# Kernel optimization log

Measured on AMD Instinct MI355X. Metric: run time of the kernel, lower is better.

Reference implementation:

```python
import jax, jax.numpy as jnp
import numpy as np

N_NODES = 100000
N_EDGES = 800000
IN_DIM = 128
HIDDEN_DIM = 256
OUT_DIM = 40


def setup_inputs() -> dict:
    key = jax.random.key(0)
    k_x, k_e, k_w1, k_w2 = jax.random.split(key, 4)
    x = jax.random.normal(k_x, (N_NODES, IN_DIM), dtype=jnp.float32)
    edge_index = jax.random.randint(k_e, (2, N_EDGES), 0, N_NODES, dtype=jnp.int32)
    # Glorot-style init like PyG GCNConv
    s1 = 1.0 / np.sqrt(IN_DIM)
    s2 = 1.0 / np.sqrt(HIDDEN_DIM)
    W1 = jax.random.uniform(k_w1, (IN_DIM, HIDDEN_DIM), dtype=jnp.float32, minval=-s1, maxval=s1)
    b1 = jnp.zeros((HIDDEN_DIM,), dtype=jnp.float32)
    W2 = jax.random.uniform(k_w2, (HIDDEN_DIM, OUT_DIM), dtype=jnp.float32, minval=-s2, maxval=s2)
    b2 = jnp.zeros((OUT_DIM,), dtype=jnp.float32)
    return {"x": x, "edge_index": edge_index, "W1": W1, "b1": b1, "W2": W2, "b2": b2}


def _gcn_conv(x, W, b, src, dst, n_nodes):
    # PyG GCNConv: linear transform, add self-loops, symmetric normalization,
    # scatter-add aggregation, then bias.
    h = x @ W  # [N, F_out]
    loops = jnp.arange(n_nodes, dtype=src.dtype)
    s = jnp.concatenate([src, loops])  # [E+N]
    d = jnp.concatenate([dst, loops])
    deg = jax.ops.segment_sum(jnp.ones_like(d, dtype=h.dtype), d, num_segments=n_nodes)
    dinv = jax.lax.rsqrt(jnp.maximum(deg, 1.0))  # deg >= 1 with self-loops
    norm = dinv[s] * dinv[d]  # [E+N]
    msgs = h[s] * norm[:, None]  # [E+N, F_out] -- dominant memory traffic
    out = jax.ops.segment_sum(msgs, d, num_segments=n_nodes)
    return out + b


def reference(x, edge_index, W1, b1, W2, b2):
    src, dst = edge_index[0], edge_index[1]
    n = x.shape[0]
    h = _gcn_conv(x, W1, b1, src, dst, n)
    h = jax.nn.relu(h)
    # dropout is identity in eval mode
    h = _gcn_conv(h, W2, b2, src, dst, n)
    return jax.nn.log_softmax(h, axis=1)
```

## Files before the change

### kernel.cpp

```cpp
#include <hip/hip_runtime.h>
#include <math.h>

#define N_NODES 100000
#define N_EDGES 800000
#define IN_DIM 128
#define HIDDEN_DIM 256
#define OUT_DIM 40
#define CAP 32
#define SHARD_DIV 12500
#define NPAIRS (N_NODES * 64)
#define T1 (HIDDEN_DIM * IN_DIM)
#define T2 (64 * HIDDEN_DIM)
#define CHUNKS 782
#define GROUP 40
#define NBLOCKS (CHUNKS * GROUP)

typedef __attribute__((ext_vector_type(8))) __bf16 bf16x8;
typedef __attribute__((ext_vector_type(4))) float f32x4;

#define FIXSC 131072.0f
#define FIXSC_INV 7.62939453125e-6f

__device__ __forceinline__ unsigned short f2bf(float f) {
    unsigned u = __float_as_uint(f);
    unsigned r = (u + 0x7FFFu + ((u >> 16) & 1u)) >> 16;
    return (unsigned short)r;
}
__device__ __forceinline__ float bflo(unsigned v) { return __uint_as_float(v << 16); }
__device__ __forceinline__ float bfhi(unsigned v) { return __uint_as_float(v & 0xFFFF0000u); }

__device__ __forceinline__ bf16x8 ld_frag16(const unsigned short* p) {
    union { uint4 u; bf16x8 b; } t;
    t.u = *(const uint4*)p;
    return t.b;
}

__global__ __launch_bounds__(256) void fillcast_kernel(const int* __restrict__ src,
                                                       const int* __restrict__ dst,
                                                       int* __restrict__ cnt,
                                                       int* __restrict__ esrc,
                                                       const float* __restrict__ x,
                                                       unsigned* __restrict__ xs,
                                                       const float* __restrict__ W1,
                                                       unsigned short* __restrict__ W1t,
                                                       const float* __restrict__ W2,
                                                       unsigned short* __restrict__ W2f) {
    int bid = blockIdx.x;
    int g = bid / GROUP, r = bid % GROUP;
    if (r < 8) {
        int lo = r * SHARD_DIV;
        int i0 = g * 1024 + threadIdx.x * 4;
        if (i0 + 3 < N_EDGES) {
            int4 d4 = *(const int4*)&dst[i0];
            if ((unsigned)(d4.x - lo) < (unsigned)SHARD_DIV) {
                int p = atomicAdd(&cnt[d4.x], 1);
                if (p < CAP) esrc[d4.x * CAP + p] = src[i0];
            }
            if ((unsigned)(d4.y - lo) < (unsigned)SHARD_DIV) {
                int p = atomicAdd(&cnt[d4.y], 1);
                if (p < CAP) esrc[d4.y * CAP + p] = src[i0 + 1];
            }
            if ((unsigned)(d4.z - lo) < (unsigned)SHARD_DIV) {
                int p = atomicAdd(&cnt[d4.z], 1);
                if (p < CAP) esrc[d4.z * CAP + p] = src[i0 + 2];
            }
            if ((unsigned)(d4.w - lo) < (unsigned)SHARD_DIV) {
                int p = atomicAdd(&cnt[d4.w], 1);
                if (p < CAP) esrc[d4.w * CAP + p] = src[i0 + 3];
            }
        } else {
            for (int j = 0; j < 4; j++) {
                int i = i0 + j;
                if (i < N_EDGES) {
                    int d = dst[i];
                    if ((unsigned)(d - lo) < (unsigned)SHARD_DIV) {
                        int p = atomicAdd(&cnt[d], 1);
                        if (p < CAP) esrc[d * CAP + p] = src[i];
                    }
                }
            }
        }
    } else {
        int ci = g * 32 + (r - 8);
        int i = ci * 256 + threadIdx.x;
        if (i < NPAIRS) {
            float2 v = ((const float2*)x)[i];
            xs[i] = (unsigned)f2bf(v.x * FIXSC) | ((unsigned)f2bf(v.y * FIXSC) << 16);
        }
        if (i < T1) {
            int n = i >> 7, k = i & 127;
            W1t[i] = f2bf(W1[(size_t)k * HIDDEN_DIM + n]);
        } else if (i < T1 + T2) {
            int j = i - T1;
            int e = j & 7, lane = (j >> 3) & 63, frag = j >> 9;
            int l16 = lane & 15, quad = lane >> 4;
            int c2 = frag >> 3, chunk = (frag >> 1) & 3, kk = frag & 1;
            int n = c2 * 16 + l16;
            int k = chunk * 64 + kk * 32 + quad * 8 + e;
            float v = (n < OUT_DIM) ? W2[(size_t)k * OUT_DIM + n] : 0.0f;
            W2f[j] = f2bf(v);
        }
    }
}

__global__ __launch_bounds__(256) void aggx_kernel(const unsigned* __restrict__ xs,
                                                   const int* __restrict__ cnt,
                                                   const int* __restrict__ esrc,
                                                   unsigned* __restrict__ aggxb, int n) {
    int wave = (blockIdx.x * 256 + threadIdx.x) >> 6;
    int lane = threadIdx.x & 63;
    int half = lane >> 5, l32 = lane & 31;
    int node = wave * 2 + half;
    if (node >= n) return;
    int c = cnt[node];
    int m = c < CAP ? c : CAP;
    const uint2* xs2 = (const uint2*)xs;
    float dn = rsqrtf((float)c + 1.0f);
    uint2 v = xs2[(size_t)node * 32 + l32];
    int ia0 = (int)(bflo(v.x) * dn), ib0 = (int)(bfhi(v.x) * dn);
    int ia1 = (int)(bflo(v.y) * dn), ib1 = (int)(bfhi(v.y) * dn);
    int base = node * CAP;
    int j = 0;
    for (; j + 7 < m; j += 8) {
        int4 sa = *(const int4*)&esrc[base + j];
        int4 sb = *(const int4*)&esrc[base + j + 4];
        float d0 = rsqrtf((float)cnt[sa.x] + 1.0f);
        float d1 = rsqrtf((float)cnt[sa.y] + 1.0f);
        float d2 = rsqrtf((float)cnt[sa.z] + 1.0f);
        float d3 = rsqrtf((float)cnt[sa.w] + 1.0f);
        float d4 = rsqrtf((float)cnt[sb.x] + 1.0f);
        float d5 = rsqrtf((float)cnt[sb.y] + 1.0f);
        float d6 = rsqrtf((float)cnt[sb.z] + 1.0f);
        float d7 = rsqrtf((float)cnt[sb.w] + 1.0f);
        uint2 u0 = xs2[(size_t)sa.x * 32 + l32];
        uint2 u1 = xs2[(size_t)sa.y * 32 + l32];
        uint2 u2 = xs2[(size_t)sa.z * 32 + l32];
        uint2 u3 = xs2[(size_t)sa.w * 32 + l32];
        uint2 u4 = xs2[(size_t)sb.x * 32 + l32];
        uint2 u5 = xs2[(size_t)sb.y * 32 + l32];
        uint2 u6 = xs2[(size_t)sb.z * 32 + l32];
        uint2 u7 = xs2[(size_t)sb.w * 32 + l32];
        ia0 += ((int)(bflo(u0.x) * d0) + (int)(bflo(u1.x) * d1)) + ((int)(bflo(u2.x) * d2) + (int)(bflo(u3.x) * d3))
             + ((int)(bflo(u4.x) * d4) + (int)(bflo(u5.x) * d5)) + ((int)(bflo(u6.x) * d6) + (int)(bflo(u7.x) * d7));
        ib0 += ((int)(bfhi(u0.x) * d0) + (int)(bfhi(u1.x) * d1)) + ((int)(bfhi(u2.x) * d2) + (int)(bfhi(u3.x) * d3))
             + ((int)(bfhi(u4.x) * d4) + (int)(bfhi(u5.x) * d5)) + ((int)(bfhi(u6.x) * d6) + (int)(bfhi(u7.x) * d7));
        ia1 += ((int)(bflo(u0.y) * d0) + (int)(bflo(u1.y) * d1)) + ((int)(bflo(u2.y) * d2) + (int)(bflo(u3.y) * d3))
             + ((int)(bflo(u4.y) * d4) + (int)(bflo(u5.y) * d5)) + ((int)(bflo(u6.y) * d6) + (int)(bflo(u7.y) * d7));
        ib1 += ((int)(bfhi(u0.y) * d0) + (int)(bfhi(u1.y) * d1)) + ((int)(bfhi(u2.y) * d2) + (int)(bfhi(u3.y) * d3))
             + ((int)(bfhi(u4.y) * d4) + (int)(bfhi(u5.y) * d5)) + ((int)(bfhi(u6.y) * d6) + (int)(bfhi(u7.y) * d7));
    }
    for (; j + 3 < m; j += 4) {
        int4 s = *(const int4*)&esrc[base + j];
        float d0 = rsqrtf((float)cnt[s.x] + 1.0f);
        float d1 = rsqrtf((float)cnt[s.y] + 1.0f);
        float d2 = rsqrtf((float)cnt[s.z] + 1.0f);
        float d3 = rsqrtf((float)cnt[s.w] + 1.0f);
        uint2 u0 = xs2[(size_t)s.x * 32 + l32];
        uint2 u1 = xs2[(size_t)s.y * 32 + l32];
        uint2 u2 = xs2[(size_t)s.z * 32 + l32];
        uint2 u3 = xs2[(size_t)s.w * 32 + l32];
        ia0 += ((int)(bflo(u0.x) * d0) + (int)(bflo(u1.x) * d1)) + ((int)(bflo(u2.x) * d2) + (int)(bflo(u3.x) * d3));
        ib0 += ((int)(bfhi(u0.x) * d0) + (int)(bfhi(u1.x) * d1)) + ((int)(bfhi(u2.x) * d2) + (int)(bfhi(u3.x) * d3));
        ia1 += ((int)(bflo(u0.y) * d0) + (int)(bflo(u1.y) * d1)) + ((int)(bflo(u2.y) * d2) + (int)(bflo(u3.y) * d3));
        ib1 += ((int)(bfhi(u0.y) * d0) + (int)(bfhi(u1.y) * d1)) + ((int)(bfhi(u2.y) * d2) + (int)(bfhi(u3.y) * d3));
    }
    for (; j < m; j++) {
        int s = esrc[base + j];
        float d = rsqrtf((float)cnt[s] + 1.0f);
        uint2 u = xs2[(size_t)s * 32 + l32];
        ia0 += (int)(bflo(u.x) * d); ib0 += (int)(bfhi(u.x) * d);
        ia1 += (int)(bflo(u.y) * d); ib1 += (int)(bfhi(u.y) * d);
    }
    float k = dn * FIXSC_INV;
    uint2 o;
    o.x = (unsigned)f2bf((float)ia0 * k) | ((unsigned)f2bf((float)ib0 * k) << 16);
    o.y = (unsigned)f2bf((float)ia1 * k) | ((unsigned)f2bf((float)ib1 * k) << 16);
    ((uint2*)aggxb)[(size_t)node * 32 + l32] = o;
}

#define BSTR 136
#define HSTR 72
__device__ __forceinline__ void phase2_epi(f32x4 (&acc)[16], int rowg,
                                           unsigned short* hw,
                                           const unsigned short* __restrict__ W2f,
                                           const float* __restrict__ b1,
                                           const int* __restrict__ cnt,
                                           unsigned short* __restrict__ h2s,
                                           int lane, int quad, int l16, int M) {
    f32x4 acc2[3];
#pragma unroll
    for (int c2 = 0; c2 < 3; c2++) acc2[c2] = (f32x4){0.f, 0.f, 0.f, 0.f};
#pragma unroll
    for (int chunk = 0; chunk < 4; chunk++) {
#pragma unroll
        for (int cc = 0; cc < 4; cc++) {
            int ct = chunk * 4 + cc;
            float bb = b1[ct * 16 + l16];
#pragma unroll
            for (int r = 0; r < 4; r++) {
                int row = quad * 4 + r;
                float v = fmaxf(acc[ct][r] + bb, 0.0f);
                hw[row * HSTR + cc * 16 + l16] = f2bf(v);
            }
        }
#pragma unroll
        for (int kk = 0; kk < 2; kk++) {
            bf16x8 af2 = ld_frag16(&hw[l16 * HSTR + kk * 32 + quad * 8]);
#pragma unroll
            for (int c2 = 0; c2 < 3; c2++) {
                bf16x8 bfr = ld_frag16(&W2f[(size_t)((c2 * 8 + chunk * 2 + kk) * 64 + lane) * 8]);
                acc2[c2] = __builtin_amdgcn_mfma_f32_16x16x32_bf16(af2, bfr, acc2[c2], 0, 0, 0);
            }
        }
    }
#pragma unroll
    for (int c2 = 0; c2 < 3; c2++) {
        int col = c2 * 16 + l16;
#pragma unroll
        for (int r = 0; r < 4; r++) {
            int gm = rowg + quad * 4 + r;
            if (gm < M) {
                float v = acc2[c2][r] * (rsqrtf((float)cnt[gm] + 1.0f) * FIXSC);
                h2s[(size_t)gm * 64 + col] = f2bf(v);
            }
        }
    }
}

__global__ __launch_bounds__(256, 2) void gemm12_kernel(const unsigned short* __restrict__ A,
                                                        const unsigned short* __restrict__ W1t,
                                                        const unsigned short* __restrict__ W2f,
                                                        const float* __restrict__ b1,
                                                        const int* __restrict__ cnt,
                                                        unsigned short* __restrict__ h2s,
                                                        int M) {
    __shared__ __align__(16) unsigned short Bs[256 * BSTR];
    __shared__ __align__(16) unsigned short Hs[4 * 16 * HSTR];
    int tid = threadIdx.x;
    int wv = tid >> 6, lane = tid & 63;
    int quad = lane >> 4, l16 = lane & 15;
    int row0 = blockIdx.x * 128 + wv * 32;

#pragma unroll
    for (int rep = 0; rep < 16; rep++) {
        int lin = rep * 256 + tid;
        int row = lin >> 4, ch = lin & 15;
        *(uint4*)&Bs[row * BSTR + ch * 8] = *(const uint4*)&W1t[(size_t)row * 128 + ch * 8];
    }

    f32x4 zero4 = {0.f, 0.f, 0.f, 0.f};
    f32x4 accA[16], accB[16];
#pragma unroll
    for (int ct = 0; ct < 16; ct++) { accA[ct] = zero4; accB[ct] = zero4; }

    __syncthreads();

#pragma unroll
    for (int k0 = 0; k0 < 128; k0 += 32) {
        int gmA = row0 + l16, gmB = row0 + 16 + l16;
        union { uint4 u; bf16x8 b; } cvA, cvB;
        cvA.u = make_uint4(0u, 0u, 0u, 0u);
        cvB.u = make_uint4(0u, 0u, 0u, 0u);
        if (gmA < M) cvA.u = *(const uint4*)&A[(size_t)gmA * 128 + k0 + quad * 8];
        if (gmB < M) cvB.u = *(const uint4*)&A[(size_t)gmB * 128 + k0 + quad * 8];
#pragma unroll
        for (int ct = 0; ct < 16; ct++) {
            bf16x8 bfr = ld_frag16(&Bs[(ct * 16 + l16) * BSTR + k0 + quad * 8]);
            accA[ct] = __builtin_amdgcn_mfma_f32_16x16x32_bf16(cvA.b, bfr, accA[ct], 0, 0, 0);
            accB[ct] = __builtin_amdgcn_mfma_f32_16x16x32_bf16(cvB.b, bfr, accB[ct], 0, 0, 0);
        }
    }

    unsigned short* hw = &Hs[wv * 16 * HSTR];
    phase2_epi(accA, row0,      hw, W2f, b1, cnt, h2s, lane, quad, l16, M);
    phase2_epi(accB, row0 + 16, hw, W2f, b1, cnt, h2s, lane, quad, l16, M);
}

__global__ __launch_bounds__(256) void agg2_kernel(const unsigned* __restrict__ h2u,
                                                   const int* __restrict__ cnt,
                                                   const int* __restrict__ esrc,
                                                   const float* __restrict__ b2,
                                                   float* __restrict__ out, int n) {
    int wave = (blockIdx.x * 256 + threadIdx.x) >> 6;
    int lane = threadIdx.x & 63;
    int half = lane >> 5, l32 = lane & 31;
    int node = wave * 2 + half;
    if (node >= n) return;
    int c = cnt[node];
    int m = c < CAP ? c : CAP;
    int base = node * CAP;
    unsigned v = h2u[(size_t)node * 32 + l32];
    int ia = (int)bflo(v), ib = (int)bfhi(v);
    int j = 0;
    for (; j + 7 < m; j += 8) {
        int s0 = esrc[base + j],     s1 = esrc[base + j + 1];
        int s2 = esrc[base + j + 2], s3 = esrc[base + j + 3];
        int s4 = esrc[base + j + 4], s5 = esrc[base + j + 5];
        int s6 = esrc[base + j + 6], s7 = esrc[base + j + 7];
        unsigned u0 = h2u[(size_t)s0 * 32 + l32];
        unsigned u1 = h2u[(size_t)s1 * 32 + l32];
        unsigned u2 = h2u[(size_t)s2 * 32 + l32];
        unsigned u3 = h2u[(size_t)s3 * 32 + l32];
        unsigned u4 = h2u[(size_t)s4 * 32 + l32];
        unsigned u5 = h2u[(size_t)s5 * 32 + l32];
        unsigned u6 = h2u[(size_t)s6 * 32 + l32];
        unsigned u7 = h2u[(size_t)s7 * 32 + l32];
        ia += ((int)bflo(u0) + (int)bflo(u1)) + ((int)bflo(u2) + (int)bflo(u3))
            + ((int)bflo(u4) + (int)bflo(u5)) + ((int)bflo(u6) + (int)bflo(u7));
        ib += ((int)bfhi(u0) + (int)bfhi(u1)) + ((int)bfhi(u2) + (int)bfhi(u3))
            + ((int)bfhi(u4) + (int)bfhi(u5)) + ((int)bfhi(u6) + (int)bfhi(u7));
    }
    for (; j + 3 < m; j += 4) {
        int s0 = esrc[base + j],     s1 = esrc[base + j + 1];
        int s2 = esrc[base + j + 2], s3 = esrc[base + j + 3];
        unsigned u0 = h2u[(size_t)s0 * 32 + l32];
        unsigned u1 = h2u[(size_t)s1 * 32 + l32];
        unsigned u2 = h2u[(size_t)s2 * 32 + l32];
        unsigned u3 = h2u[(size_t)s3 * 32 + l32];
        ia += ((int)bflo(u0) + (int)bflo(u1)) + ((int)bflo(u2) + (int)bflo(u3));
        ib += ((int)bfhi(u0) + (int)bfhi(u1)) + ((int)bfhi(u2) + (int)bfhi(u3));
    }
    for (; j < m; j++) {
        unsigned u = h2u[(size_t)esrc[base + j] * 32 + l32];
        ia += (int)bflo(u); ib += (int)bfhi(u);
    }
    float k = rsqrtf((float)c + 1.0f) * FIXSC_INV;
    int f0 = 2 * l32;
    bool a0 = (f0 < OUT_DIM), a1 = (f0 + 1 < OUT_DIM);
    float v0 = a0 ? fmaf((float)ia, k, b2[f0]) : -INFINITY;
    float v1 = a1 ? fmaf((float)ib, k, b2[f0 + 1]) : -INFINITY;
    float mx = fmaxf(v0, v1);
#pragma unroll
    for (int o = 16; o > 0; o >>= 1) mx = fmaxf(mx, __shfl_xor(mx, o));
    float e = (a0 ? __expf(v0 - mx) : 0.0f) + (a1 ? __expf(v1 - mx) : 0.0f);
#pragma unroll
    for (int o = 16; o > 0; o >>= 1) e += __shfl_xor(e, o);
    if (a0) {
        float ls = __logf(e);
        *(float2*)&out[(size_t)node * OUT_DIM + f0] = make_float2(v0 - mx - ls, v1 - mx - ls);
    }
}

extern "C" void kernel_launch(void* const* d_in, const int* in_sizes, int n_in,
                              void* d_out, int out_size, void* d_ws, size_t ws_size,
                              hipStream_t stream) {
    const float* x  = (const float*)d_in[0];
    const int* ei   = (const int*)d_in[1];
    const float* W1 = (const float*)d_in[2];
    const float* b1 = (const float*)d_in[3];
    const float* W2 = (const float*)d_in[4];
    const float* b2 = (const float*)d_in[5];
    float* out = (float*)d_out;

    const int* src = ei;
    const int* dst = ei + N_EDGES;

    char* ws = (char*)d_ws;
    size_t off = 0;
    auto carve = [&](size_t bytes) -> char* {
        char* p = ws + off;
        off = (off + bytes + 255) & ~(size_t)255;
        return p;
    };
    int*      cnt   = (int*)     carve((size_t)N_NODES * 4);
    int*      esrc  = (int*)     carve((size_t)N_NODES * CAP * 4);
    unsigned* xs    = (unsigned*)carve((size_t)N_NODES * 64 * 4);
    unsigned short* W1t = (unsigned short*)carve((size_t)T1 * 2);
    unsigned short* W2f = (unsigned short*)carve((size_t)T2 * 2);
    unsigned* aggxb = (unsigned*)carve((size_t)N_NODES * 64 * 4);
    unsigned short* h2s = (unsigned short*)carve((size_t)N_NODES * 64 * 2);

    hipMemsetAsync(cnt, 0, (size_t)N_NODES * 4, stream);
    fillcast_kernel<<<NBLOCKS, 256, 0, stream>>>(
        src, dst, cnt, esrc, x, xs, W1, W1t, W2, W2f);
    aggx_kernel<<<((N_NODES + 1) / 2 * 64 + 255) / 256, 256, 0, stream>>>(
        xs, cnt, esrc, aggxb, N_NODES);
    gemm12_kernel<<<(N_NODES + 127) / 128, 256, 0, stream>>>(
        (const unsigned short*)aggxb, W1t, W2f, b1, cnt, h2s, N_NODES);
    agg2_kernel<<<((N_NODES + 1) / 2 * 64 + 255) / 256, 256, 0, stream>>>(
        (const unsigned*)h2s, cnt, esrc, b2, out, N_NODES);
}
```

Before: 241.1 us.

## Precompute degree-inverse array and read W1 fragments directly from global memory

Adds a small kernel that computes rsqrt(deg+1) once per node into a float array, and the aggregation and GEMM kernels now load it instead of recomputing rsqrt from counts. The GEMM kernel also stops staging W1 into a large shared-memory tile and drops the barrier, reading B fragments straight from global memory (cache-resident). This lowers LDS use, which may raise occupancy, and removes repeated rsqrt work. In exchange it adds an extra launch and uncoalesced global fragment loads inside the MFMA loop.

```diff
diff --git a/kernel.cpp b/kernel.cpp
--- a/kernel.cpp
+++ b/kernel.cpp
@@ -103,8 +103,15 @@
     }
 }
 
+__global__ __launch_bounds__(256) void dinv_kernel(const int* __restrict__ cnt,
+                                                   float* __restrict__ dinvf, int n) {
+    int i = blockIdx.x * 256 + threadIdx.x;
+    if (i < n) dinvf[i] = rsqrtf((float)cnt[i] + 1.0f);
+}
+
 __global__ __launch_bounds__(256) void aggx_kernel(const unsigned* __restrict__ xs,
                                                    const int* __restrict__ cnt,
+                                                   const float* __restrict__ dinvf,
                                                    const int* __restrict__ esrc,
                                                    unsigned* __restrict__ aggxb, int n) {
     int wave = (blockIdx.x * 256 + threadIdx.x) >> 6;
@@ -115,7 +122,7 @@
     int c = cnt[node];
     int m = c < CAP ? c : CAP;
     const uint2* xs2 = (const uint2*)xs;
-    float dn = rsqrtf((float)c + 1.0f);
+    float dn = dinvf[node];
     uint2 v = xs2[(size_t)node * 32 + l32];
     int ia0 = (int)(bflo(v.x) * dn), ib0 = (int)(bfhi(v.x) * dn);
     int ia1 = (int)(bflo(v.y) * dn), ib1 = (int)(bfhi(v.y) * dn);
@@ -124,14 +131,14 @@
     for (; j + 7 < m; j += 8) {
         int4 sa = *(const int4*)&esrc[base + j];
         int4 sb = *(const int4*)&esrc[base + j + 4];
-        float d0 = rsqrtf((float)cnt[sa.x] + 1.0f);
-        float d1 = rsqrtf((float)cnt[sa.y] + 1.0f);
-        float d2 = rsqrtf((float)cnt[sa.z] + 1.0f);
-        float d3 = rsqrtf((float)cnt[sa.w] + 1.0f);
-        float d4 = rsqrtf((float)cnt[sb.x] + 1.0f);
-        float d5 = rsqrtf((float)cnt[sb.y] + 1.0f);
-        float d6 = rsqrtf((float)cnt[sb.z] + 1.0f);
-        float d7 = rsqrtf((float)cnt[sb.w] + 1.0f);
+        float d0 = dinvf[sa.x];
+        float d1 = dinvf[sa.y];
+        float d2 = dinvf[sa.z];
+        float d3 = dinvf[sa.w];
+        float d4 = dinvf[sb.x];
+        float d5 = dinvf[sb.y];
+        float d6 = dinvf[sb.z];
+        float d7 = dinvf[sb.w];
         uint2 u0 = xs2[(size_t)sa.x * 32 + l32];
         uint2 u1 = xs2[(size_t)sa.y * 32 + l32];
         uint2 u2 = xs2[(size_t)sa.z * 32 + l32];
@@ -151,10 +158,10 @@
     }
     for (; j + 3 < m; j += 4) {
         int4 s = *(const int4*)&esrc[base + j];
-        float d0 = rsqrtf((float)cnt[s.x] + 1.0f);
-        float d1 = rsqrtf((float)cnt[s.y] + 1.0f);
-        float d2 = rsqrtf((float)cnt[s.z] + 1.0f);
-        float d3 = rsqrtf((float)cnt[s.w] + 1.0f);
+        float d0 = dinvf[s.x];
+        float d1 = dinvf[s.y];
+        float d2 = dinvf[s.z];
+        float d3 = dinvf[s.w];
         uint2 u0 = xs2[(size_t)s.x * 32 + l32];
         uint2 u1 = xs2[(size_t)s.y * 32 + l32];
         uint2 u2 = xs2[(size_t)s.z * 32 + l32];
@@ -166,7 +173,7 @@
     }
     for (; j < m; j++) {
         int s = esrc[base + j];
-        float d = rsqrtf((float)cnt[s] + 1.0f);
+        float d = dinvf[s];
         uint2 u = xs2[(size_t)s * 32 + l32];
         ia0 += (int)(bflo(u.x) * d); ib0 += (int)(bfhi(u.x) * d);
         ia1 += (int)(bflo(u.y) * d); ib1 += (int)(bfhi(u.y) * d);
@@ -178,13 +185,12 @@
     ((uint2*)aggxb)[(size_t)node * 32 + l32] = o;
 }
 
-#define BSTR 136
 #define HSTR 72
 __device__ __forceinline__ void phase2_epi(f32x4 (&acc)[16], int rowg,
                                            unsigned short* hw,
                                            const unsigned short* __restrict__ W2f,
                                            const float* __restrict__ b1,
-                                           const int* __restrict__ cnt,
+                                           const float* __restrict__ dinvf,
                                            unsigned short* __restrict__ h2s,
                                            int lane, int quad, int l16, int M) {
     f32x4 acc2[3];
@@ -220,7 +226,7 @@
         for (int r = 0; r < 4; r++) {
             int gm = rowg + quad * 4 + r;
             if (gm < M) {
-                float v = acc2[c2][r] * (rsqrtf((float)cnt[gm] + 1.0f) * FIXSC);
+                float v = acc2[c2][r] * (dinvf[gm] * FIXSC);
                 h2s[(size_t)gm * 64 + col] = f2bf(v);
             }
         }
@@ -231,29 +237,19 @@
                                                         const unsigned short* __restrict__ W1t,
                                                         const unsigned short* __restrict__ W2f,
                                                         const float* __restrict__ b1,
-                                                        const int* __restrict__ cnt,
+                                                        const float* __restrict__ dinvf,
                                                         unsigned short* __restrict__ h2s,
                                                         int M) {
-    __shared__ __align__(16) unsigned short Bs[256 * BSTR];
     __shared__ __align__(16) unsigned short Hs[4 * 16 * HSTR];
     int tid = threadIdx.x;
     int wv = tid >> 6, lane = tid & 63;
     int quad = lane >> 4, l16 = lane & 15;
     int row0 = blockIdx.x * 128 + wv * 32;
 
-#pragma unroll
-    for (int rep = 0; rep < 16; rep++) {
-        int lin = rep * 256 + tid;
-        int row = lin >> 4, ch = lin & 15;
-        *(uint4*)&Bs[row * BSTR + ch * 8] = *(const uint4*)&W1t[(size_t)row * 128 + ch * 8];
-    }
-
     f32x4 zero4 = {0.f, 0.f, 0.f, 0.f};
     f32x4 accA[16], accB[16];
 #pragma unroll
     for (int ct = 0; ct < 16; ct++) { accA[ct] = zero4; accB[ct] = zero4; }
-
-    __syncthreads();
 
 #pragma unroll
     for (int k0 = 0; k0 < 128; k0 += 32) {
@@ -265,19 +261,20 @@
         if (gmB < M) cvB.u = *(const uint4*)&A[(size_t)gmB * 128 + k0 + quad * 8];
 #pragma unroll
         for (int ct = 0; ct < 16; ct++) {
-            bf16x8 bfr = ld_frag16(&Bs[(ct * 16 + l16) * BSTR + k0 + quad * 8]);
+            bf16x8 bfr = ld_frag16(&W1t[(size_t)(ct * 16 + l16) * 128 + k0 + quad * 8]);
             accA[ct] = __builtin_amdgcn_mfma_f32_16x16x32_bf16(cvA.b, bfr, accA[ct], 0, 0, 0);
             accB[ct] = __builtin_amdgcn_mfma_f32_16x16x32_bf16(cvB.b, bfr, accB[ct], 0, 0, 0);
         }
     }
 
     unsigned short* hw = &Hs[wv * 16 * HSTR];
-    phase2_epi(accA, row0,      hw, W2f, b1, cnt, h2s, lane, quad, l16, M);
-    phase2_epi(accB, row0 + 16, hw, W2f, b1, cnt, h2s, lane, quad, l16, M);
+    phase2_epi(accA, row0,      hw, W2f, b1, dinvf, h2s, lane, quad, l16, M);
+    phase2_epi(accB, row0 + 16, hw, W2f, b1, dinvf, h2s, lane, quad, l16, M);
 }
 
 __global__ __launch_bounds__(256) void agg2_kernel(const unsigned* __restrict__ h2u,
                                                    const int* __restrict__ cnt,
+                                                   const float* __restrict__ dinvf,
                                                    const int* __restrict__ esrc,
                                                    const float* __restrict__ b2,
                                                    float* __restrict__ out, int n) {
@@ -324,7 +321,7 @@
         unsigned u = h2u[(size_t)esrc[base + j] * 32 + l32];
         ia += (int)bflo(u); ib += (int)bfhi(u);
     }
-    float k = rsqrtf((float)c + 1.0f) * FIXSC_INV;
+    float k = dinvf[node] * FIXSC_INV;
     int f0 = 2 * l32;
     bool a0 = (f0 < OUT_DIM), a1 = (f0 + 1 < OUT_DIM);
     float v0 = a0 ? fmaf((float)ia, k, b2[f0]) : -INFINITY;
@@ -369,14 +366,16 @@
     unsigned short* W2f = (unsigned short*)carve((size_t)T2 * 2);
     unsigned* aggxb = (unsigned*)carve((size_t)N_NODES * 64 * 4);
     unsigned short* h2s = (unsigned short*)carve((size_t)N_NODES * 64 * 2);
+    float*    dinvf = (float*)   carve((size_t)N_NODES * 4);
 
     hipMemsetAsync(cnt, 0, (size_t)N_NODES * 4, stream);
     fillcast_kernel<<<NBLOCKS, 256, 0, stream>>>(
         src, dst, cnt, esrc, x, xs, W1, W1t, W2, W2f);
+    dinv_kernel<<<(N_NODES + 255) / 256, 256, 0, stream>>>(cnt, dinvf, N_NODES);
     aggx_kernel<<<((N_NODES + 1) / 2 * 64 + 255) / 256, 256, 0, stream>>>(
-        xs, cnt, esrc, aggxb, N_NODES);
+        xs, cnt, dinvf, esrc, aggxb, N_NODES);
     gemm12_kernel<<<(N_NODES + 127) / 128, 256, 0, stream>>>(
-        (const unsigned short*)aggxb, W1t, W2f, b1, cnt, h2s, N_NODES);
+        (const unsigned short*)aggxb, W1t, W2f, b1, dinvf, h2s, N_NODES);
     agg2_kernel<<<((N_NODES + 1) / 2 * 64 + 255) / 256, 256, 0, stream>>>(
-        (const unsigned*)h2s, cnt, esrc, b2, out, N_NODES);
-}
+        (const unsigned*)h2s, cnt, dinvf, esrc, b2, out, N_NODES);
+}
```

After: 273.6 us. +13.5%, slower.
